# Kernel optimization log

Measured on AMD Instinct MI355X. Metric: run time of the kernel, lower is better.

The kernel has to match this reference:

```python
import jax, jax.numpy as jnp
import numpy as np
import math

B, T, C, H = 2, 2048, 1024, 16
D = C // H
EPS = 1e-5

def _layer_norm(x, w, b):
    m = jnp.mean(x, axis=-1, keepdims=True)
    v = jnp.mean((x - m) ** 2, axis=-1, keepdims=True)
    return (x - m) * jax.lax.rsqrt(v + EPS) * w + b

def setup_inputs() -> dict:
    key = jax.random.key(0)
    ks = jax.random.split(key, 8)
    s_attn = 1.0 / math.sqrt(C)
    s_fc = 1.0 / math.sqrt(C)
    s_fc2 = 1.0 / math.sqrt(4 * C)
    return {
        "x": jax.random.normal(ks[0], (B, T, C), dtype=jnp.float32),
        "ln1_w": jnp.ones((C,), jnp.float32),
        "ln1_b": jnp.zeros((C,), jnp.float32),
        "w_qkv": jax.random.normal(ks[1], (C, 3 * C), jnp.float32) * s_attn,  # [in,out]
        "b_qkv": jnp.zeros((3 * C,), jnp.float32),
        "w_proj": jax.random.normal(ks[2], (C, C), jnp.float32) * s_attn,
        "b_proj": jnp.zeros((C,), jnp.float32),
        "ln2_w": jnp.ones((C,), jnp.float32),
        "ln2_b": jnp.zeros((C,), jnp.float32),
        "w_fc": jax.random.normal(ks[3], (C, 4 * C), jnp.float32) * s_fc,
        "b_fc": jnp.zeros((4 * C,), jnp.float32),
        "w_fc2": jax.random.normal(ks[4], (4 * C, C), jnp.float32) * s_fc2,
        "b_fc2": jnp.zeros((C,), jnp.float32),
    }

def reference(x, ln1_w, ln1_b, w_qkv, b_qkv, w_proj, b_proj,
              ln2_w, ln2_b, w_fc, b_fc, w_fc2, b_fc2):
    # --- attention branch ---
    h = _layer_norm(x, ln1_w, ln1_b)
    qkv = h @ w_qkv + b_qkv                      # [B,T,3C]
    q, k, v = jnp.split(qkv, 3, axis=-1)
    # [B,T,C] -> [B,H,T,D]
    q = q.reshape(B, T, H, D).transpose(0, 2, 1, 3)
    k = k.reshape(B, T, H, D).transpose(0, 2, 1, 3)
    v = v.reshape(B, T, H, D).transpose(0, 2, 1, 3)
    scale = 1.0 / math.sqrt(D)
    scores = jnp.einsum("bhtd,bhsd->bhts", q, k) * scale  # [B,H,T,T]
    causal = jnp.tril(jnp.ones((T, T), dtype=bool))
    scores = jnp.where(causal, scores, -jnp.inf)
    attn_w = jax.nn.softmax(scores, axis=-1)     # dropout_p = 0.0
    attn_out = jnp.einsum("bhts,bhsd->bhtd", attn_w, v)
    attn_out = attn_out.transpose(0, 2, 1, 3).reshape(B, T, C)
    attn_out = attn_out @ w_proj + b_proj
    x = x + attn_out
    # --- MLP branch ---
    h2 = _layer_norm(x, ln2_w, ln2_b)
    h2 = jax.nn.gelu(h2 @ w_fc + b_fc, approximate=False)
    x = x + (h2 @ w_fc2 + b_fc2)
    return x, jnp.mean(attn_w, axis=0)           # ([B,T,C], [H,T,T])
```

## Files before the change

### kernel.cpp

```cpp
#include <hip/hip_runtime.h>
#include <cmath>

#define BB 2
#define TT 2048
#define CC 1024
#define HH 16
#define DD 64

typedef unsigned short u16;
typedef __attribute__((ext_vector_type(8))) short bf16x8;
typedef __attribute__((ext_vector_type(8))) _Float16 f16x8;
typedef __attribute__((ext_vector_type(4))) float f32x4;

__device__ __forceinline__ u16 f2bf(float f) {
    union { float f; unsigned u; } v; v.f = f;
    return (u16)((v.u + 0x7fff + ((v.u >> 16) & 1)) >> 16);
}

__device__ __forceinline__ u16 f2h(float f) {
    union { _Float16 h; u16 u; } v; v.h = (_Float16)f;
    return v.u;
}

__device__ __forceinline__ float fexp2(float x) {
    float r; asm("v_exp_f32 %0, %1" : "=v"(r) : "v"(x)); return r;
}

__device__ __forceinline__ float gelu_exact(float v) {
    return 0.5f * v * (1.0f + erff(v * 0.70710678118654752440f));
}

__device__ __forceinline__ void glds16(const void* g, void* l) {
    __builtin_amdgcn_global_load_lds(
        (const __attribute__((address_space(1))) void*)g,
        (__attribute__((address_space(3))) void*)l, 16, 0, 0);
}

__global__ __launch_bounds__(256) void wcvt_kernel(const float* __restrict__ W,
                                                   u16* __restrict__ WT,
                                                   int K, int N) {
    __shared__ u16 t[64][65];
    const int n0 = blockIdx.x * 64, k0 = blockIdx.y * 64;
    const int tid = threadIdx.x;
    const int c = tid & 63;
#pragma unroll
    for (int it = 0; it < 16; ++it) {
        int r = it * 4 + (tid >> 6);
        t[c][r] = f2bf(W[(size_t)(k0 + r) * N + n0 + c]);
    }
    __syncthreads();
#pragma unroll
    for (int it = 0; it < 16; ++it) {
        int r = it * 4 + (tid >> 6);
        WT[(size_t)(n0 + r) * K + k0 + c] = t[r][c];
    }
}

__global__ __launch_bounds__(256) void ln_kernel(const float* __restrict__ x,
                                                 const float* __restrict__ w,
                                                 const float* __restrict__ b,
                                                 u16* __restrict__ out) {
    const int tid = threadIdx.x;
    const int lane = tid & 63;
    const int row = blockIdx.x * 4 + (tid >> 6);
    const float* xr = x + (size_t)row * CC;
    u16* orow = out + (size_t)row * CC;

    float4 v[4];
#pragma unroll
    for (int k = 0; k < 4; ++k)
        v[k] = *reinterpret_cast<const float4*>(xr + k * 256 + lane * 4);

    float s = 0.f;
#pragma unroll
    for (int k = 0; k < 4; ++k) s += v[k].x + v[k].y + v[k].z + v[k].w;
#pragma unroll
    for (int off = 1; off < 64; off <<= 1) s += __shfl_xor(s, off);
    const float mean = s * (1.0f / CC);

    float sq = 0.f;
#pragma unroll
    for (int k = 0; k < 4; ++k) {
        float dx = v[k].x - mean, dy = v[k].y - mean, dz = v[k].z - mean, dw = v[k].w - mean;
        sq += dx * dx + dy * dy + dz * dz + dw * dw;
    }
#pragma unroll
    for (int off = 1; off < 64; off <<= 1) sq += __shfl_xor(sq, off);
    const float rstd = rsqrtf(sq * (1.0f / CC) + 1e-5f);

#pragma unroll
    for (int k = 0; k < 4; ++k) {
        const int c = k * 256 + lane * 4;
        float4 w4 = *reinterpret_cast<const float4*>(w + c);
        float4 b4 = *reinterpret_cast<const float4*>(b + c);
        ushort4 o = make_ushort4(f2bf((v[k].x - mean) * rstd * w4.x + b4.x),
                                 f2bf((v[k].y - mean) * rstd * w4.y + b4.y),
                                 f2bf((v[k].z - mean) * rstd * w4.z + b4.z),
                                 f2bf((v[k].w - mean) * rstd * w4.w + b4.w));
        *reinterpret_cast<ushort4*>(orow + c) = o;
    }
}

template <int EPI, int OUTBF, int WM, int WN, int FI, int FJ>
__global__ __launch_bounds__(512) void gemm_mfma(const u16* __restrict__ A,
                                                 const u16* __restrict__ BT,
                                                 const float* __restrict__ bias,
                                                 const float* __restrict__ res,
                                                 void* __restrict__ out,
                                                 u16* __restrict__ kh,
                                                 u16* __restrict__ vh,
                                                 int M, int N, int K) {
    constexpr int TM = WM * FI * 16;
    constexpr int TN = WN * FJ * 16;
    __shared__ u16 As[2][TM * 64];
    __shared__ u16 Bs[2][TN * 64];

    const int tid = threadIdx.x;
    const int lane = tid & 63;
    const int w = tid >> 6;
    const int wr = w / WN, wc = w % WN;
    const int m16 = lane & 15;
    const int quad = lane >> 4;

    const int bm = blockIdx.y * TM;
    const int bn = blockIdx.x * TN;

    auto stage = [&](int buf, int kt) {
        const int k0 = kt * 64;
#pragma unroll
        for (int it = 0; it < TM / 64; ++it) {
            int c = w * (TM / 64) + it;
            int q = c * 64 + lane;
            int row = q >> 3;
            int col = ((q & 7) ^ (row & 7)) * 8;
            glds16(&A[(size_t)(bm + row) * K + k0 + col], &As[buf][c * 512]);
        }
#pragma unroll
        for (int it = 0; it < TN / 64; ++it) {
            int c = w * (TN / 64) + it;
            int q = c * 64 + lane;
            int row = q >> 3;
            int col = ((q & 7) ^ (row & 7)) * 8;
            glds16(&BT[(size_t)(bn + row) * K + k0 + col], &Bs[buf][c * 512]);
        }
    };

    f32x4 acc[FI][FJ] = {};
    const int NT = K >> 6;
    stage(0, 0);
    __syncthreads();
    int cur = 0;
    for (int kt = 0; kt < NT; ++kt) {
        if (kt + 1 < NT) stage(cur ^ 1, kt + 1);
#pragma unroll
        for (int ks = 0; ks < 2; ++ks) {
            const int co = (ks * 32 + quad * 8) ^ ((m16 & 7) << 3);
            bf16x8 a[FI], b[FJ];
#pragma unroll
            for (int i = 0; i < FI; ++i)
                a[i] = *(const bf16x8*)&As[cur][(wr * FI * 16 + 16 * i + m16) * 64 + co];
#pragma unroll
            for (int j = 0; j < FJ; ++j)
                b[j] = *(const bf16x8*)&Bs[cur][(wc * FJ * 16 + 16 * j + m16) * 64 + co];
#pragma unroll
            for (int i = 0; i < FI; ++i)
#pragma unroll
                for (int j = 0; j < FJ; ++j)
                    acc[i][j] = __builtin_amdgcn_mfma_f32_16x16x32_bf16(a[i], b[j], acc[i][j], 0, 0, 0);
        }
        __syncthreads();
        cur ^= 1;
    }

#pragma unroll
    for (int i = 0; i < FI; ++i) {
        const int row = bm + wr * FI * 16 + 16 * i + quad * 4;
#pragma unroll
        for (int j = 0; j < FJ; ++j) {
            const int col = bn + wc * FJ * 16 + 16 * j + m16;
            const float bv = bias[col];
#pragma unroll
            for (int r = 0; r < 4; ++r) {
                float v = acc[i][j][r] + bv;
                if (EPI == 1) v = gelu_exact(v);
                if (EPI == 2) v += res[(size_t)(row + r) * N + col];
                if (EPI == 3) {
                    if (col < CC) ((float*)out)[(size_t)(row + r) * CC + col] = v;
                    else if (col < 2 * CC) kh[(size_t)(row + r) * CC + (col - CC)] = f2h(v);
                    else vh[(size_t)(row + r) * CC + (col - 2 * CC)] = f2h(v);
                } else if (OUTBF) {
                    ((u16*)out)[(size_t)(row + r) * N + col] = f2bf(v);
                } else {
                    ((float*)out)[(size_t)(row + r) * N + col] = v;
                }
            }
        }
    }
}

__global__ __launch_bounds__(256) void vtr_kernel(const u16* __restrict__ Vh,
                                                  u16* __restrict__ VTt) {
    const int t0 = blockIdx.x * 64;
    const int h = blockIdx.y;
    const int b = blockIdx.z;
    const int tid = threadIdx.x;
    __shared__ u16 tl[64][65];
#pragma unroll
    for (int it = 0; it < 4; ++it) {
        int e = tid + it * 256;
        int r = e >> 4, c4 = (e & 15) * 4;
        ushort4 v = *reinterpret_cast<const ushort4*>(
            &Vh[(size_t)(b * TT + t0 + r) * CC + h * DD + c4]);
        tl[c4 + 0][r] = v.x; tl[c4 + 1][r] = v.y; tl[c4 + 2][r] = v.z; tl[c4 + 3][r] = v.w;
    }
    __syncthreads();
#pragma unroll
    for (int it = 0; it < 4; ++it) {
        int e = tid + it * 256;
        int d = e >> 4, s4 = (e & 15) * 4;
        ushort4 o = make_ushort4(tl[d][s4], tl[d][s4 + 1], tl[d][s4 + 2], tl[d][s4 + 3]);
        *reinterpret_cast<ushort4*>(&VTt[(size_t)((b * HH + h) * DD + d) * TT + t0 + s4]) = o;
    }
}

__global__ __launch_bounds__(256) void attn_kernel(const float* __restrict__ Qf,
                                                   const u16* __restrict__ Kh,
                                                   const u16* __restrict__ VTt,
                                                   float* __restrict__ attn_mean,
                                                   u16* __restrict__ attn_out) {
    const int lid = blockIdx.x;
    const int u = lid & 255;
    const int h = u & 15;
    const int ta = u >> 4;
    const int tt = (lid < 256) ? ta : 31 - ta;
    const int t0 = tt * 64;

    const int tid = threadIdx.x;
    const int lane = tid & 63;
    const int w = tid >> 6;
    const int m16 = lane & 15;
    const int quad = lane >> 4;

    __shared__ u16 smem[2][4][4096];
    __shared__ u16 Pm[2][4096];

    const int arow = w * 16 + m16;
    const int sw = (m16 & 7) << 3;
    const int rbase = w * 16 + quad * 4;

    auto KSL = [&](int buf, int b) -> const u16 (*)[64] { return (const u16(*)[64]) & smem[buf][b][0]; };
    auto VSL = [&](int buf, int b) -> const u16 (*)[64] { return (const u16(*)[64]) & smem[buf][2 + b][0]; };

    auto stage_K = [&](int buf, int b, int st) {
#pragma unroll
        for (int it = 0; it < 2; ++it) {
            int c = w * 2 + it;
            int s = c * 8 + (lane >> 3);
            int scol = ((lane & 7) * 8) ^ ((s & 7) << 3);
            glds16(&Kh[(size_t)(b * TT + st * 64 + s) * CC + h * DD + scol],
                   &smem[buf][b][c * 512]);
        }
    };
    auto stage_V = [&](int buf, int b, int st) {
#pragma unroll
        for (int it = 0; it < 2; ++it) {
            int c = w * 2 + it;
            int d = c * 8 + (lane >> 3);
            int scol = ((lane & 7) * 8) ^ ((d & 7) << 3);
            glds16(&VTt[(size_t)((b * HH + h) * DD + d) * TT + st * 64 + scol],
                   &smem[buf][2 + b][c * 512]);
        }
    };
    auto stage_K2 = [&](int buf, int st) { stage_K(buf, 0, st); stage_K(buf, 1, st); };
    auto stage_KV4 = [&](int buf, int st) {
        stage_K2(buf, st); stage_V(buf, 0, st); stage_V(buf, 1, st);
    };

    const float QSCALE = 0.125f * 1.4426950408889634f;
    f16x8 qh[2][2];
#pragma unroll
    for (int b = 0; b < 2; ++b) {
        const float* qp = Qf + (size_t)(b * TT + t0 + arow) * CC + h * DD;
#pragma unroll
        for (int ks = 0; ks < 2; ++ks) {
            float4 v0 = *reinterpret_cast<const float4*>(qp + ks * 32 + quad * 8);
            float4 v1 = *reinterpret_cast<const float4*>(qp + ks * 32 + quad * 8 + 4);
            float f[8] = {v0.x, v0.y, v0.z, v0.w, v1.x, v1.y, v1.z, v1.w};
            union { f16x8 v; u16 s[8]; } H;
#pragma unroll
            for (int i = 0; i < 8; ++i) H.s[i] = f2h(f[i] * QSCALE);
            qh[b][ks] = H.v;
        }
    }

    auto compute_S = [&](const f16x8 (&QH)[2], const u16 (*KT)[64],
                         f32x4 (&acc)[4], bool diag) {
        __builtin_amdgcn_s_setprio(1);
#pragma unroll
        for (int ks = 0; ks < 2; ++ks) {
            const int co = (ks * 32 + quad * 8) ^ sw;
#pragma unroll
            for (int j = 0; j < 4; ++j) {
                f16x8 bh = *(const f16x8*)&KT[j * 16 + m16][co];
                acc[j] = __builtin_amdgcn_mfma_f32_16x16x32_f16(QH[ks], bh, acc[j], 0, 0, 0);
            }
        }
        __builtin_amdgcn_s_setprio(0);
        if (diag) {
#pragma unroll
            for (int j = 0; j < 4; ++j)
#pragma unroll
                for (int r = 0; r < 4; ++r)
                    if (j * 16 + m16 > rbase + r) acc[j][r] = -INFINITY;
        }
    };

    auto pv_acc = [&](f32x4 (&O)[4], const u16* Pp, const u16 (*VT)[64]) {
        __builtin_amdgcn_s_setprio(1);
#pragma unroll
        for (int ks = 0; ks < 2; ++ks) {
            const int co = (ks * 32 + quad * 8) ^ sw;
            f16x8 a = *(const f16x8*)&Pp[arow * 64 + co];
#pragma unroll
            for (int j = 0; j < 4; ++j) {
                f16x8 bv = *(const f16x8*)&VT[j * 16 + m16][co];
                O[j] = __builtin_amdgcn_mfma_f32_16x16x32_f16(a, bv, O[j], 0, 0, 0);
            }
        }
        __builtin_amdgcn_s_setprio(0);
    };

    float l_r[2][4] = {};
    stage_K2(0, 0);
    for (int st = 0; st <= tt; ++st) {
        const int cur = st & 1;
        __syncthreads();
        if (st + 1 <= tt) stage_K2(cur ^ 1, st + 1);
        const bool diag = (st == tt);
#pragma unroll
        for (int b = 0; b < 2; ++b) {
            f32x4 acc[4] = {};
            compute_S(qh[b], KSL(cur, b), acc, diag);
#pragma unroll
            for (int r = 0; r < 4; ++r)
                l_r[b][r] += (fexp2(acc[0][r]) + fexp2(acc[1][r])) +
                             (fexp2(acc[2][r]) + fexp2(acc[3][r]));
        }
    }
    __syncthreads();
#pragma unroll
    for (int b = 0; b < 2; ++b)
#pragma unroll
        for (int r = 0; r < 4; ++r) {
            float s = l_r[b][r];
            s += __shfl_xor(s, 1);
            s += __shfl_xor(s, 2);
            s += __shfl_xor(s, 4);
            s += __shfl_xor(s, 8);
            l_r[b][r] = 1.0f / s;
        }

    f32x4 O0[4] = {}, O1[4] = {};
    stage_KV4(0, 0);
    for (int st = 0; st <= tt; ++st) {
        const int cur = st & 1;
        const int s0 = st * 64;
        const bool diag = (st == tt);
        __syncthreads();
        if (st + 1 <= tt) stage_KV4(cur ^ 1, st + 1);

        f32x4 a0[4] = {}, a1[4] = {};
        compute_S(qh[0], KSL(cur, 0), a0, diag);
        compute_S(qh[1], KSL(cur, 1), a1, diag);

#pragma unroll
        for (int j = 0; j < 4; ++j)
#pragma unroll
            for (int r = 0; r < 4; ++r) {
                a0[j][r] = fexp2(a0[j][r]) * l_r[0][r];
                a1[j][r] = fexp2(a1[j][r]) * l_r[1][r];
            }

#pragma unroll
        for (int r = 0; r < 4; ++r) {
            float* mrow = attn_mean + ((size_t)h * TT + t0 + rbase + r) * TT + s0;
#pragma unroll
            for (int j = 0; j < 4; ++j)
                mrow[j * 16 + m16] = 0.5f * (a0[j][r] + a1[j][r]);
        }

#pragma unroll
        for (int r = 0; r < 4; ++r) {
            const int prow = rbase + r;
            const int psw = (prow & 7) << 3;
#pragma unroll
            for (int j = 0; j < 4; ++j) {
                Pm[0][prow * 64 + ((j * 16 + m16) ^ psw)] = f2h(a0[j][r]);
                Pm[1][prow * 64 + ((j * 16 + m16) ^ psw)] = f2h(a1[j][r]);
            }
        }
        pv_acc(O0, &Pm[0][0], VSL(cur, 0));
        pv_acc(O1, &Pm[1][0], VSL(cur, 1));
    }

#pragma unroll
    for (int r = 0; r < 4; ++r) {
        const int trow = t0 + rbase + r;
#pragma unroll
        for (int j = 0; j < 4; ++j) {
            attn_out[((size_t)0 * TT + trow) * CC + h * DD + j * 16 + m16] = f2bf(O0[j][r]);
            attn_out[((size_t)1 * TT + trow) * CC + h * DD + j * 16 + m16] = f2bf(O1[j][r]);
        }
    }

    const int c0 = (tt + 1) * 64;
    const float4 z4 = make_float4(0.f, 0.f, 0.f, 0.f);
    for (int r = 0; r < 64; ++r) {
        float* row = attn_mean + ((size_t)h * TT + t0 + r) * TT;
        for (int c = c0 + tid * 4; c < TT; c += 1024)
            *reinterpret_cast<float4*>(row + c) = z4;
    }
}

extern "C" void kernel_launch(void* const* d_in, const int* in_sizes, int n_in,
                              void* d_out, int out_size, void* d_ws, size_t ws_size,
                              hipStream_t stream) {
    const float* x      = (const float*)d_in[0];
    const float* ln1_w  = (const float*)d_in[1];
    const float* ln1_b  = (const float*)d_in[2];
    const float* w_qkv  = (const float*)d_in[3];
    const float* b_qkv  = (const float*)d_in[4];
    const float* w_proj = (const float*)d_in[5];
    const float* b_proj = (const float*)d_in[6];
    const float* ln2_w  = (const float*)d_in[7];
    const float* ln2_b  = (const float*)d_in[8];
    const float* w_fc   = (const float*)d_in[9];
    const float* b_fc   = (const float*)d_in[10];
    const float* w_fc2  = (const float*)d_in[11];
    const float* b_fc2  = (const float*)d_in[12];

    float* out_x    = (float*)d_out;
    float* out_attn = out_x + (size_t)BB * TT * CC;

    char* wp = (char*)d_ws;
    u16* wT_qkv = (u16*)wp;  wp += (size_t)3072 * 1024 * 2;
    u16* wT_proj = (u16*)wp; wp += (size_t)1024 * 1024 * 2;
    u16* wT_fc  = (u16*)wp;  wp += (size_t)4096 * 1024 * 2;
    u16* wT_fc2 = (u16*)wp;  wp += (size_t)1024 * 4096 * 2;
    u16* h_ln   = (u16*)wp;  wp += (size_t)4096 * 1024 * 2;
    u16* att_o  = (u16*)wp;  wp += (size_t)4096 * 1024 * 2;
    u16* h2     = (u16*)wp;  wp += (size_t)4096 * 4096 * 2;
    float* Qf   = (float*)wp; wp += (size_t)4096 * 1024 * 4;
    float* x1   = (float*)wp; wp += (size_t)4096 * 1024 * 4;

    u16* Kh  = h2;
    u16* Vh  = Kh + (size_t)4096 * 1024;
    u16* VTt = Vh + (size_t)4096 * 1024;

    const int M = BB * TT;

    wcvt_kernel<<<dim3(3072 / 64, 1024 / 64), 256, 0, stream>>>(w_qkv, wT_qkv, 1024, 3072);
    wcvt_kernel<<<dim3(1024 / 64, 1024 / 64), 256, 0, stream>>>(w_proj, wT_proj, 1024, 1024);
    wcvt_kernel<<<dim3(4096 / 64, 1024 / 64), 256, 0, stream>>>(w_fc, wT_fc, 1024, 4096);
    wcvt_kernel<<<dim3(1024 / 64, 4096 / 64), 256, 0, stream>>>(w_fc2, wT_fc2, 4096, 1024);

    ln_kernel<<<M / 4, 256, 0, stream>>>(x, ln1_w, ln1_b, h_ln);
    gemm_mfma<3, 0, 2, 4, 8, 2><<<dim3(3072 / 128, M / 256), 512, 0, stream>>>(
        h_ln, wT_qkv, b_qkv, nullptr, Qf, Kh, Vh, M, 3072, 1024);
    vtr_kernel<<<dim3(TT / 64, HH, BB), 256, 0, stream>>>(Vh, VTt);
    attn_kernel<<<512, 256, 0, stream>>>(Qf, Kh, VTt, out_attn, att_o);
    gemm_mfma<2, 0, 2, 4, 4, 2><<<dim3(1024 / 128, M / 128), 512, 0, stream>>>(
        att_o, wT_proj, b_proj, x, x1, nullptr, nullptr, M, 1024, 1024);
    ln_kernel<<<M / 4, 256, 0, stream>>>(x1, ln2_w, ln2_b, h_ln);
    gemm_mfma<1, 1, 2, 4, 8, 2><<<dim3(4096 / 128, M / 256), 512, 0, stream>>>(
        h_ln, wT_fc, b_fc, nullptr, h2, nullptr, nullptr, M, 4096, 1024);
    gemm_mfma<2, 0, 2, 4, 4, 2><<<dim3(1024 / 128, M / 128), 512, 0, stream>>>(
        h2, wT_fc2, b_fc2, x1, out_x, nullptr, nullptr, M, 1024, 4096);
}
```

Before: 678.5 us.

## Use 256x256 tiles for wide GEMMs and small-tile single-buffer GEMM for narrow ones

The QKV and FC GEMMs move to a 256x256 tile (8x4 MFMA fragments per wave) with s_setprio raised around the MFMA burst. The proj and FC2 GEMMs (N=1024) switch to a new 256-thread kernel with 128x64 tiles and a single LDS buffer, which gives more blocks across the CUs. Larger tiles cut global and LDS traffic per FLOP but raise register pressure and reduce the block count. The narrow GEMMs give up double buffering in exchange for better occupancy.

```diff
diff --git a/kernel.cpp b/kernel.cpp
--- a/kernel.cpp
+++ b/kernel.cpp
@@ -101,24 +101,22 @@
     }
 }
 
-template <int EPI, int OUTBF, int WM, int WN, int FI, int FJ>
-__global__ __launch_bounds__(512) void gemm_mfma(const u16* __restrict__ A,
-                                                 const u16* __restrict__ BT,
-                                                 const float* __restrict__ bias,
-                                                 const float* __restrict__ res,
-                                                 void* __restrict__ out,
-                                                 u16* __restrict__ kh,
-                                                 u16* __restrict__ vh,
-                                                 int M, int N, int K) {
-    constexpr int TM = WM * FI * 16;
-    constexpr int TN = WN * FJ * 16;
+template <int EPI>
+__global__ __launch_bounds__(512, 2) void gemm_db(const u16* __restrict__ A,
+                                                  const u16* __restrict__ BT,
+                                                  const float* __restrict__ bias,
+                                                  void* __restrict__ out,
+                                                  u16* __restrict__ kh,
+                                                  u16* __restrict__ vh,
+                                                  int M, int N, int K) {
+    constexpr int TM = 256, TN = 256;
     __shared__ u16 As[2][TM * 64];
     __shared__ u16 Bs[2][TN * 64];
 
     const int tid = threadIdx.x;
     const int lane = tid & 63;
     const int w = tid >> 6;
-    const int wr = w / WN, wc = w % WN;
+    const int wr = w >> 2, wc = w & 3;
     const int m16 = lane & 15;
     const int quad = lane >> 4;
 
@@ -128,16 +126,16 @@
     auto stage = [&](int buf, int kt) {
         const int k0 = kt * 64;
 #pragma unroll
-        for (int it = 0; it < TM / 64; ++it) {
-            int c = w * (TM / 64) + it;
+        for (int it = 0; it < 4; ++it) {
+            int c = w * 4 + it;
             int q = c * 64 + lane;
             int row = q >> 3;
             int col = ((q & 7) ^ (row & 7)) * 8;
             glds16(&A[(size_t)(bm + row) * K + k0 + col], &As[buf][c * 512]);
         }
 #pragma unroll
-        for (int it = 0; it < TN / 64; ++it) {
-            int c = w * (TN / 64) + it;
+        for (int it = 0; it < 4; ++it) {
+            int c = w * 4 + it;
             int q = c * 64 + lane;
             int row = q >> 3;
             int col = ((q & 7) ^ (row & 7)) * 8;
@@ -145,7 +143,7 @@
         }
     };
 
-    f32x4 acc[FI][FJ] = {};
+    f32x4 acc[8][4] = {};
     const int NT = K >> 6;
     stage(0, 0);
     __syncthreads();
@@ -155,44 +153,118 @@
 #pragma unroll
         for (int ks = 0; ks < 2; ++ks) {
             const int co = (ks * 32 + quad * 8) ^ ((m16 & 7) << 3);
-            bf16x8 a[FI], b[FJ];
-#pragma unroll
-            for (int i = 0; i < FI; ++i)
-                a[i] = *(const bf16x8*)&As[cur][(wr * FI * 16 + 16 * i + m16) * 64 + co];
-#pragma unroll
-            for (int j = 0; j < FJ; ++j)
-                b[j] = *(const bf16x8*)&Bs[cur][(wc * FJ * 16 + 16 * j + m16) * 64 + co];
-#pragma unroll
-            for (int i = 0; i < FI; ++i)
-#pragma unroll
-                for (int j = 0; j < FJ; ++j)
+            bf16x8 a[8], b[4];
+#pragma unroll
+            for (int i = 0; i < 8; ++i)
+                a[i] = *(const bf16x8*)&As[cur][(wr * 128 + 16 * i + m16) * 64 + co];
+#pragma unroll
+            for (int j = 0; j < 4; ++j)
+                b[j] = *(const bf16x8*)&Bs[cur][(wc * 64 + 16 * j + m16) * 64 + co];
+            __builtin_amdgcn_s_setprio(1);
+#pragma unroll
+            for (int i = 0; i < 8; ++i)
+#pragma unroll
+                for (int j = 0; j < 4; ++j)
                     acc[i][j] = __builtin_amdgcn_mfma_f32_16x16x32_bf16(a[i], b[j], acc[i][j], 0, 0, 0);
+            __builtin_amdgcn_s_setprio(0);
         }
         __syncthreads();
         cur ^= 1;
     }
 
 #pragma unroll
-    for (int i = 0; i < FI; ++i) {
-        const int row = bm + wr * FI * 16 + 16 * i + quad * 4;
-#pragma unroll
-        for (int j = 0; j < FJ; ++j) {
-            const int col = bn + wc * FJ * 16 + 16 * j + m16;
+    for (int i = 0; i < 8; ++i) {
+        const int row = bm + wr * 128 + 16 * i + quad * 4;
+#pragma unroll
+        for (int j = 0; j < 4; ++j) {
+            const int col = bn + wc * 64 + 16 * j + m16;
             const float bv = bias[col];
 #pragma unroll
             for (int r = 0; r < 4; ++r) {
                 float v = acc[i][j][r] + bv;
-                if (EPI == 1) v = gelu_exact(v);
-                if (EPI == 2) v += res[(size_t)(row + r) * N + col];
-                if (EPI == 3) {
+                if (EPI == 1) {
+                    v = gelu_exact(v);
+                    ((u16*)out)[(size_t)(row + r) * N + col] = f2bf(v);
+                } else {
                     if (col < CC) ((float*)out)[(size_t)(row + r) * CC + col] = v;
                     else if (col < 2 * CC) kh[(size_t)(row + r) * CC + (col - CC)] = f2h(v);
                     else vh[(size_t)(row + r) * CC + (col - 2 * CC)] = f2h(v);
-                } else if (OUTBF) {
-                    ((u16*)out)[(size_t)(row + r) * N + col] = f2bf(v);
-                } else {
-                    ((float*)out)[(size_t)(row + r) * N + col] = v;
                 }
+            }
+        }
+    }
+}
+
+__global__ __launch_bounds__(256) void gemm_sm(const u16* __restrict__ A,
+                                               const u16* __restrict__ BT,
+                                               const float* __restrict__ bias,
+                                               const float* __restrict__ res,
+                                               float* __restrict__ out,
+                                               int M, int N, int K) {
+    constexpr int TM = 128, TN = 64;
+    __shared__ u16 As[TM * 64];
+    __shared__ u16 Bs[TN * 64];
+
+    const int tid = threadIdx.x;
+    const int lane = tid & 63;
+    const int w = tid >> 6;
+    const int m16 = lane & 15;
+    const int quad = lane >> 4;
+
+    const int bm = blockIdx.y * TM;
+    const int bn = blockIdx.x * TN;
+
+    f32x4 acc[2][4] = {};
+
+    for (int k0 = 0; k0 < K; k0 += 64) {
+#pragma unroll
+        for (int it = 0; it < 4; ++it) {
+            int c = w * 4 + it;
+            int q = c * 64 + lane;
+            int row = q >> 3;
+            int col = ((q & 7) ^ (row & 7)) * 8;
+            glds16(&A[(size_t)(bm + row) * K + k0 + col], &As[c * 512]);
+        }
+#pragma unroll
+        for (int it = 0; it < 2; ++it) {
+            int c = w * 2 + it;
+            int q = c * 64 + lane;
+            int row = q >> 3;
+            int col = ((q & 7) ^ (row & 7)) * 8;
+            glds16(&BT[(size_t)(bn + row) * K + k0 + col], &Bs[c * 512]);
+        }
+        __syncthreads();
+
+#pragma unroll
+        for (int ks = 0; ks < 2; ++ks) {
+            const int co = (ks * 32 + quad * 8) ^ ((m16 & 7) << 3);
+            bf16x8 a[2], b[4];
+#pragma unroll
+            for (int i = 0; i < 2; ++i)
+                a[i] = *(const bf16x8*)&As[(w * 32 + 16 * i + m16) * 64 + co];
+#pragma unroll
+            for (int j = 0; j < 4; ++j)
+                b[j] = *(const bf16x8*)&Bs[(16 * j + m16) * 64 + co];
+#pragma unroll
+            for (int i = 0; i < 2; ++i)
+#pragma unroll
+                for (int j = 0; j < 4; ++j)
+                    acc[i][j] = __builtin_amdgcn_mfma_f32_16x16x32_bf16(a[i], b[j], acc[i][j], 0, 0, 0);
+        }
+        __syncthreads();
+    }
+
+#pragma unroll
+    for (int i = 0; i < 2; ++i) {
+        const int row = bm + w * 32 + 16 * i + quad * 4;
+#pragma unroll
+        for (int j = 0; j < 4; ++j) {
+            const int col = bn + 16 * j + m16;
+            const float bv = bias[col];
+#pragma unroll
+            for (int r = 0; r < 4; ++r) {
+                float v = acc[i][j][r] + bv + res[(size_t)(row + r) * N + col];
+                out[(size_t)(row + r) * N + col] = v;
             }
         }
     }
@@ -465,15 +537,15 @@
     wcvt_kernel<<<dim3(1024 / 64, 4096 / 64), 256, 0, stream>>>(w_fc2, wT_fc2, 4096, 1024);
 
     ln_kernel<<<M / 4, 256, 0, stream>>>(x, ln1_w, ln1_b, h_ln);
-    gemm_mfma<3, 0, 2, 4, 8, 2><<<dim3(3072 / 128, M / 256), 512, 0, stream>>>(
-        h_ln, wT_qkv, b_qkv, nullptr, Qf, Kh, Vh, M, 3072, 1024);
+    gemm_db<3><<<dim3(3072 / 256, M / 256), 512, 0, stream>>>(
+        h_ln, wT_qkv, b_qkv, Qf, Kh, Vh, M, 3072, 1024);
     vtr_kernel<<<dim3(TT / 64, HH, BB), 256, 0, stream>>>(Vh, VTt);
     attn_kernel<<<512, 256, 0, stream>>>(Qf, Kh, VTt, out_attn, att_o);
-    gemm_mfma<2, 0, 2, 4, 4, 2><<<dim3(1024 / 128, M / 128), 512, 0, stream>>>(
-        att_o, wT_proj, b_proj, x, x1, nullptr, nullptr, M, 1024, 1024);
+    gemm_sm<<<dim3(1024 / 64, M / 128), 256, 0, stream>>>(
+        att_o, wT_proj, b_proj, x, x1, M, 1024, 1024);
     ln_kernel<<<M / 4, 256, 0, stream>>>(x1, ln2_w, ln2_b, h_ln);
-    gemm_mfma<1, 1, 2, 4, 8, 2><<<dim3(4096 / 128, M / 256), 512, 0, stream>>>(
-        h_ln, wT_fc, b_fc, nullptr, h2, nullptr, nullptr, M, 4096, 1024);
-    gemm_mfma<2, 0, 2, 4, 4, 2><<<dim3(1024 / 128, M / 128), 512, 0, stream>>>(
-        h2, wT_fc2, b_fc2, x1, out_x, nullptr, nullptr, M, 1024, 4096);
-}
+    gemm_db<1><<<dim3(4096 / 256, M / 256), 512, 0, stream>>>(
+        h_ln, wT_fc, b_fc, h2, nullptr, nullptr, M, 4096, 1024);
+    gemm_sm<<<dim3(1024 / 64, M / 128), 256, 0, stream>>>(
+        h2, wT_fc2, b_fc2, x1, out_x, M, 1024, 4096);
+}
```

Result: faster. 644.8 us (-5.0%).
